# Kernel tuning notes

Hardware: AMD Instinct MI355X
Metric: run time of the kernel (lower is better)

The kernel has to match this reference:

```python
import jax, jax.numpy as jnp
import numpy as np

HEAD = 64

PARAM_NAMES = ['x_r','x_w','x_k','x_v','x_a','x_g','w0','w1','w2','a0','a1','a2',
               'v0','v1','v2','g1','g2','k_k','k_a','r_k','W_r','W_k','W_v','W_o',
               'ln_x_w','ln_x_b','ln1_w','ln1_b','ln2_w','ln2_b','c_x_k','W_ck','W_cv']


def token_shift(x):
    # previous token, zero-padded at t=0 (stateless shift state)
    return jnp.pad(x, ((0, 0), (1, 0), (0, 0)))[:, :-1]


def layer_norm(x, w, b, eps=1e-5):
    m = jnp.mean(x, -1, keepdims=True)
    v = jnp.mean(jnp.square(x - m), -1, keepdims=True)
    return (x - m) * jax.lax.rsqrt(v + eps) * w + b


def group_norm_heads(x, w, b, H, eps=64e-5):
    # GroupNorm(H, C) as used by RWKV7 ln_x (eps = head_size * 1e-5)
    B, T, C = x.shape
    xh = x.reshape(B, T, H, C // H)
    m = jnp.mean(xh, -1, keepdims=True)
    v = jnp.mean(jnp.square(xh - m), -1, keepdims=True)
    xh = (xh - m) * jax.lax.rsqrt(v + eps)
    return xh.reshape(B, T, C) * w + b


def wkv7(r, w, k, v, a, b):
    # r,w,k,v,a,b: [B,T,H,N]; w is per-channel decay in (0,1)
    # S_t = S_{t-1} * diag(w_t) + (S_{t-1} @ a_t) b_t^T + v_t k_t^T ; y_t = S_t @ r_t
    B, T, H, N = r.shape
    def step(S, inp):
        r_t, w_t, k_t, v_t, a_t, b_t = inp
        sa = jnp.einsum('bhij,bhj->bhi', S, a_t)
        S = S * w_t[:, :, None, :] + sa[..., None] * b_t[:, :, None, :] + v_t[..., None] * k_t[:, :, None, :]
        y = jnp.einsum('bhij,bhj->bhi', S, r_t)
        return S, y
    xs = tuple(jnp.moveaxis(t, 1, 0) for t in (r, w, k, v, a, b))
    S0 = jnp.zeros((B, H, N, N), r.dtype)
    _, ys = jax.lax.scan(step, S0, xs)
    return jnp.moveaxis(ys, 0, 1)


def time_mix(x, v_first, p, is_first_layer):
    B, T, C = x.shape
    H, N = C // HEAD, HEAD
    xx = token_shift(x) - x
    xr = x + xx * p['x_r']; xw = x + xx * p['x_w']; xk = x + xx * p['x_k']
    xv = x + xx * p['x_v']; xa = x + xx * p['x_a']; xg = x + xx * p['x_g']
    r = xr @ p['W_r']
    w = -jax.nn.softplus(-(p['w0'] + jnp.tanh(xw @ p['w1']) @ p['w2'])) - 0.5
    k = xk @ p['W_k']
    v = xv @ p['W_v']
    if is_first_layer:
        v_first = v
    else:
        v = v + (v_first - v) * jax.nn.sigmoid(p['v0'] + (xv @ p['v1']) @ p['v2'])
    a = jax.nn.sigmoid(p['a0'] + (xa @ p['a1']) @ p['a2'])  # in-context learning rate
    g = jax.nn.sigmoid(xg @ p['g1']) @ p['g2']
    kk = (k * p['k_k']).reshape(B, T, H, N)
    kk = kk / jnp.maximum(jnp.linalg.norm(kk, axis=-1, keepdims=True), 1e-12)
    k = k * (1.0 + (a - 1.0) * p['k_a'])
    decay = jnp.exp(-jnp.exp(w)).reshape(B, T, H, N)
    rh = r.reshape(B, T, H, N)
    kh = k.reshape(B, T, H, N)
    vh = v.reshape(B, T, H, N)
    ah = a.reshape(B, T, H, N)
    y = wkv7(rh, decay, kh, vh, -kk, kk * ah).reshape(B, T, C)
    y = group_norm_heads(y, p['ln_x_w'], p['ln_x_b'], H)
    bonus = jnp.sum(rh * kh * p['r_k'], -1, keepdims=True) * vh
    y = y + bonus.reshape(B, T, C)
    return (y * g) @ p['W_o'], v_first


def channel_mix(x, p):
    xx = token_shift(x) - x
    k = x + xx * p['c_x_k']
    k = jnp.square(jax.nn.relu(k @ p['W_ck']))
    return k @ p['W_cv']


def encoder_forward(x, params):
    L = params['W_r'].shape[0]
    v_first = None
    for i in range(L):
        p = {n: params[n][i] for n in PARAM_NAMES}
        att, v_first = time_mix(layer_norm(x, p['ln1_w'], p['ln1_b']), v_first, p, i == 0)
        x = x + att
        x = x + channel_mix(layer_norm(x, p['ln2_w'], p['ln2_b']), p)
    return x


def setup_inputs() -> dict:
    key = jax.random.key(0)
    L, B, T, C = 6, 2, 512, 768
    H, N = C // HEAD, HEAD
    Dw, Da, Dv, Dg, F = 64, 64, 32, 128, 4 * C
    keys = iter(jax.random.split(key, 48))
    def rn(shape, s):
        return jax.random.normal(next(keys), shape, jnp.float32) * s
    def ru(shape):
        return jax.random.uniform(next(keys), shape, jnp.float32)
    inp = {
        'x': rn((B, T, C), 1.0),
        'x_r': ru((L, C)), 'x_w': ru((L, C)), 'x_k': ru((L, C)),
        'x_v': ru((L, C)), 'x_a': ru((L, C)), 'x_g': ru((L, C)),
        'w0': rn((L, C), 0.3), 'w1': rn((L, C, Dw), 0.02), 'w2': rn((L, Dw, C), 0.02),
        'a0': rn((L, C), 0.1), 'a1': rn((L, C, Da), 0.02), 'a2': rn((L, Da, C), 0.02),
        'v0': rn((L, C), 0.1), 'v1': rn((L, C, Dv), 0.02), 'v2': rn((L, Dv, C), 0.02),
        'g1': rn((L, C, Dg), 0.02), 'g2': rn((L, Dg, C), 0.02),
        'k_k': 0.85 + rn((L, C), 0.05), 'k_a': 1.0 + rn((L, C), 0.05),
        'r_k': rn((L, H, N), 0.1),
        'W_r': rn((L, C, C), 0.02), 'W_k': rn((L, C, C), 0.02),
        'W_v': rn((L, C, C), 0.02), 'W_o': rn((L, C, C), 0.02),
        'ln_x_w': 1.0 + rn((L, C), 0.05), 'ln_x_b': rn((L, C), 0.05),
        'ln1_w': 1.0 + rn((L, C), 0.05), 'ln1_b': rn((L, C), 0.05),
        'ln2_w': 1.0 + rn((L, C), 0.05), 'ln2_b': rn((L, C), 0.05),
        'c_x_k': ru((L, C)),
        'W_ck': rn((L, C, F), 0.02), 'W_cv': rn((L, F, C), 0.02),
    }
    return inp


def reference(x, x_r, x_w, x_k, x_v, x_a, x_g, w0, w1, w2, a0, a1, a2, v0, v1, v2,
              g1, g2, k_k, k_a, r_k, W_r, W_k, W_v, W_o, ln_x_w, ln_x_b,
              ln1_w, ln1_b, ln2_w, ln2_b, c_x_k, W_ck, W_cv):
    params = dict(zip(PARAM_NAMES, (x_r, x_w, x_k, x_v, x_a, x_g, w0, w1, w2, a0, a1, a2,
                                    v0, v1, v2, g1, g2, k_k, k_a, r_k, W_r, W_k, W_v, W_o,
                                    ln_x_w, ln_x_b, ln1_w, ln1_b, ln2_w, ln2_b, c_x_k, W_ck, W_cv)))
    return encoder_forward(x, params)
```

## Files before the change

### kernel.cpp

```cpp
#include <hip/hip_runtime.h>
#include <hip/hip_bf16.h>
#include <math.h>

#define LAYERS 6
#define BBATCH 2
#define TT 512
#define CC 768
#define HH 12
#define MT (BBATCH*TT)
#define FF (4*CC)
#define LCH 32
#define NC (TT/LCH)
#define BH (BBATCH*HH)
#define SPAD 65

typedef __hip_bfloat16 bf16;
typedef __bf16 bf16x8 __attribute__((ext_vector_type(8)));
typedef float f32x4 __attribute__((ext_vector_type(4)));

__device__ inline bf16 f2b(float f) { return __float2bfloat16(f); }


__global__ __launch_bounds__(256) void copy_f(float* __restrict__ dst, const float* __restrict__ src) {
    size_t i = (size_t)blockIdx.x * 256 + threadIdx.x;
    dst[i] = src[i];
}


__global__ __launch_bounds__(256) void ln_shift_kernel(const float* __restrict__ x,
                                                       const float* __restrict__ w,
                                                       const float* __restrict__ b,
                                                       bf16* __restrict__ out) {
    int row = blockIdx.x;
    int t = row % TT;
    const float* xr = x + (size_t)row * CC;
    const float* xp = xr - CC;
    int tid = threadIdx.x;
    float c0 = xr[tid], c1 = xr[tid + 256], c2 = xr[tid + 512];
    float p0 = 0.f, p1 = 0.f, p2 = 0.f;
    if (t > 0) { p0 = xp[tid]; p1 = xp[tid + 256]; p2 = xp[tid + 512]; }
    float s  = c0 + c1 + c2, q  = c0 * c0 + c1 * c1 + c2 * c2;
    float sp = p0 + p1 + p2, qp = p0 * p0 + p1 * p1 + p2 * p2;
    for (int m = 1; m < 64; m <<= 1) {
        s += __shfl_xor(s, m); q += __shfl_xor(q, m);
        sp += __shfl_xor(sp, m); qp += __shfl_xor(qp, m);
    }
    __shared__ float rs[4], rq[4], rsp[4], rqp[4];
    int wid = tid >> 6;
    if ((tid & 63) == 0) { rs[wid] = s; rq[wid] = q; rsp[wid] = sp; rqp[wid] = qp; }
    __syncthreads();
    s  = rs[0] + rs[1] + rs[2] + rs[3];   q  = rq[0] + rq[1] + rq[2] + rq[3];
    sp = rsp[0] + rsp[1] + rsp[2] + rsp[3]; qp = rqp[0] + rqp[1] + rqp[2] + rqp[3];
    float meanC = s * (1.f / CC);
    float invC  = rsqrtf(q * (1.f / CC) - meanC * meanC + 1e-5f);
    float meanP = sp * (1.f / CC);
    float invP  = rsqrtf(qp * (1.f / CC) - meanP * meanP + 1e-5f);
    bf16* orow = out + (size_t)row * 1536;
    float cv[3] = {c0, c1, c2};
    float pv[3] = {p0, p1, p2};
#pragma unroll
    for (int j = 0; j < 3; ++j) {
        int cc = tid + j * 256;
        float lnc = (cv[j] - meanC) * invC * w[cc] + b[cc];
        float lnp = (t > 0) ? (pv[j] - meanP) * invP * w[cc] + b[cc] : 0.f;
        orow[cc] = f2b(lnc);
        orow[768 + cc] = f2b(lnp - lnc);
    }
}


struct CEntry { const float* W; const float* mix; bf16* dst; int Ksrc, Nsrc, Npad, Kdst, bstart; };
struct CArgs { CEntry e[14]; };

__global__ __launch_bounds__(256) void convert_weights(CArgs ca) {
    int bid = blockIdx.x;
    int idx = 0;
#pragma unroll
    for (int i = 1; i < 14; ++i) if (bid >= ca.e[i].bstart) idx = i;
    CEntry E = ca.e[idx];
    int t = bid - E.bstart;
    int ntN = E.Npad >> 5;
    int tn = (t % ntN) * 32, tk = (t / ntN) * 32;
    __shared__ float tile[32][33];
    int c = threadIdx.x & 31, r0 = threadIdx.x >> 5;
    int ks = tk;
    const float* mixp = nullptr;
    if (tk >= E.Ksrc) { ks = tk - E.Ksrc; mixp = E.mix; }
#pragma unroll
    for (int i = 0; i < 4; ++i) {
        int r = r0 + i * 8;
        float v = (tn + c < E.Nsrc) ? E.W[(size_t)(ks + r) * E.Nsrc + tn + c] : 0.f;
        if (mixp) v *= mixp[ks + r];
        tile[r][c] = v;
    }
    __syncthreads();
#pragma unroll
    for (int i = 0; i < 4; ++i) {
        int r = r0 + i * 8;
        E.dst[(size_t)(tn + r) * E.Kdst + tk + c] = f2b(tile[c][r]);
    }
}


struct EpiG {
    float* outF; bf16* outH;
    const float* p1; const float* p2;
    int epi, ld, ntrue;
};
struct EpiArgs { EpiG g[7]; int nb[8]; };

__device__ inline void epi_store(const EpiG& E, size_t idx, int lc, float v) {
    switch (E.epi) {
        case 0: E.outF[idx] = v; break;
        case 1: E.outH[idx] = f2b(v); break;
        case 2: E.outH[idx] = f2b(tanhf(v)); break;
        case 3: E.outH[idx] = f2b(1.f / (1.f + expf(-v))); break;
        case 4: { float t = fmaxf(v, 0.f); E.outH[idx] = f2b(t * t); } break;
        case 5: E.outF[idx] += v; break;
        case 6: { float z = E.p1[lc] + v; float nz = -z;
                  float sp = (nz > 20.f) ? nz : log1pf(expf(nz));
                  E.outF[idx] = expf(-expf(-sp - 0.5f)); } break;
        case 7: E.outF[idx] = 1.f / (1.f + expf(-(E.p1[lc] + v))); break;
        case 8: { float vv = E.outF[idx];
                  float s = 1.f / (1.f + expf(-(E.p1[lc] + v)));
                  E.outF[idx] = vv + (E.p2[idx] - vv) * s; } break;
    }
}


template<int BM, int BN>
__global__ __launch_bounds__(256) void gemm_multi(const __bf16* __restrict__ A,
                                                  const __bf16* __restrict__ Bt,
                                                  int K, EpiArgs ea) {
    constexpr int FM = BM / 32, FN = BN / 32;
    constexpr int ABYTES = BM * 64;
    constexpr int TOT = (BM + BN) * 64;
    constexpr int NCHUNK = TOT / 4096;
    __shared__ __align__(16) char smem[2][TOT];
    int tid = threadIdx.x;
    int lane = tid & 63, wid = tid >> 6;
    int bm = blockIdx.y * BM, bn = blockIdx.x * BN;
    int wm = (wid >> 1) * (BM / 2), wn = (wid & 1) * (BN / 2);
    f32x4 acc[FM][FN];
#pragma unroll
    for (int i = 0; i < FM; ++i)
#pragma unroll
        for (int j = 0; j < FN; ++j) acc[i][j] = (f32x4){0.f, 0.f, 0.f, 0.f};

    int nk = K >> 5;
    auto stage = [&](int buf, int k0) {
        char* sb = &smem[buf][0];
#pragma unroll
        for (int c = 0; c < NCHUNK; ++c) {
            int d = c * 4096 + tid * 16;
            int isB = d >= ABYTES;
            int dd = isB ? d - ABYTES : d;
            int row = dd >> 6;
            int u = (dd >> 4) & 3;
            int su = u ^ (row & 3);
            const __bf16* src = isB ? (Bt + (size_t)(bn + row) * K + k0 + su * 8)
                                    : (A  + (size_t)(bm + row) * K + k0 + su * 8);
            char* ldst = sb + c * 4096 + (tid & 192) * 16;
            __builtin_amdgcn_global_load_lds(
                (const __attribute__((address_space(1))) unsigned int*)src,
                (__attribute__((address_space(3))) unsigned int*)ldst, 16, 0, 0);
        }
    };

    stage(0, 0);
    __syncthreads();
    for (int t = 0; t < nk; ++t) {
        if (t + 1 < nk) stage((t + 1) & 1, (t + 1) * 32);
        const char* sA = &smem[t & 1][0];
        const char* sB = &smem[t & 1][ABYTES];
        int u = lane >> 4, r0 = lane & 15;
        bf16x8 af[FM], bfr[FN];
#pragma unroll
        for (int i = 0; i < FM; ++i) {
            int row = wm + i * 16 + r0;
            int su = u ^ (row & 3);
            af[i] = *(const bf16x8*)(sA + row * 64 + su * 16);
        }
#pragma unroll
        for (int j = 0; j < FN; ++j) {
            int row = wn + j * 16 + r0;
            int su = u ^ (row & 3);
            bfr[j] = *(const bf16x8*)(sB + row * 64 + su * 16);
        }
#pragma unroll
        for (int i = 0; i < FM; ++i)
#pragma unroll
            for (int j = 0; j < FN; ++j)
                acc[i][j] = __builtin_amdgcn_mfma_f32_16x16x32_bf16(af[i], bfr[j], acc[i][j], 0, 0, 0);
        __syncthreads();
    }

    int gid = 0;
#pragma unroll 1
    while (bn >= ea.nb[gid + 1]) ++gid;
    EpiG E = ea.g[gid];
    int colBase = ea.nb[gid];
#pragma unroll
    for (int i = 0; i < FM; ++i) {
#pragma unroll
        for (int j = 0; j < FN; ++j) {
#pragma unroll
            for (int q = 0; q < 4; ++q) {
                int gm = bm + wm + i * 16 + (lane >> 4) * 4 + q;
                int lc = bn + wn + j * 16 + (lane & 15) - colBase;
                if (lc < E.ntrue)
                    epi_store(E, (size_t)gm * E.ld + lc, lc, acc[i][j][q]);
            }
        }
    }
}


struct G2G { const __bf16* A; const __bf16* Bt; float* outF; const float* p1; const float* p2; int K; int epi; };
struct G2Args { G2G g[4]; };

template<int BM, int BN>
__global__ __launch_bounds__(256) void gemm_g2(G2Args ga) {
    G2G G = ga.g[blockIdx.z];
    const __bf16* A = G.A;
    const __bf16* Bt = G.Bt;
    int K = G.K;
    constexpr int FM = BM / 32, FN = BN / 32;
    constexpr int ABYTES = BM * 64;
    constexpr int TOT = (BM + BN) * 64;
    constexpr int NCHUNK = TOT / 4096;
    __shared__ __align__(16) char smem[2][TOT];
    int tid = threadIdx.x;
    int lane = tid & 63, wid = tid >> 6;
    int bm = blockIdx.y * BM, bn = blockIdx.x * BN;
    int wm = (wid >> 1) * (BM / 2), wn = (wid & 1) * (BN / 2);
    f32x4 acc[FM][FN];
#pragma unroll
    for (int i = 0; i < FM; ++i)
#pragma unroll
        for (int j = 0; j < FN; ++j) acc[i][j] = (f32x4){0.f, 0.f, 0.f, 0.f};

    int nk = K >> 5;
    auto stage = [&](int buf, int k0) {
        char* sb = &smem[buf][0];
#pragma unroll
        for (int c = 0; c < NCHUNK; ++c) {
            int d = c * 4096 + tid * 16;
            int isB = d >= ABYTES;
            int dd = isB ? d - ABYTES : d;
            int row = dd >> 6;
            int u = (dd >> 4) & 3;
            int su = u ^ (row & 3);
            const __bf16* src = isB ? (Bt + (size_t)(bn + row) * K + k0 + su * 8)
                                    : (A  + (size_t)(bm + row) * K + k0 + su * 8);
            char* ldst = sb + c * 4096 + (tid & 192) * 16;
            __builtin_amdgcn_global_load_lds(
                (const __attribute__((address_space(1))) unsigned int*)src,
                (__attribute__((address_space(3))) unsigned int*)ldst, 16, 0, 0);
        }
    };

    stage(0, 0);
    __syncthreads();
    for (int t = 0; t < nk; ++t) {
        if (t + 1 < nk) stage((t + 1) & 1, (t + 1) * 32);
        const char* sA = &smem[t & 1][0];
        const char* sB = &smem[t & 1][ABYTES];
        int u = lane >> 4, r0 = lane & 15;
        bf16x8 af[FM], bfr[FN];
#pragma unroll
        for (int i = 0; i < FM; ++i) {
            int row = wm + i * 16 + r0;
            int su = u ^ (row & 3);
            af[i] = *(const bf16x8*)(sA + row * 64 + su * 16);
        }
#pragma unroll
        for (int j = 0; j < FN; ++j) {
            int row = wn + j * 16 + r0;
            int su = u ^ (row & 3);
            bfr[j] = *(const bf16x8*)(sB + row * 64 + su * 16);
        }
#pragma unroll
        for (int i = 0; i < FM; ++i)
#pragma unroll
            for (int j = 0; j < FN; ++j)
                acc[i][j] = __builtin_amdgcn_mfma_f32_16x16x32_bf16(af[i], bfr[j], acc[i][j], 0, 0, 0);
        __syncthreads();
    }

    EpiG E;
    E.outF = G.outF; E.outH = nullptr; E.p1 = G.p1; E.p2 = G.p2;
    E.epi = G.epi; E.ld = 768; E.ntrue = 768;
#pragma unroll
    for (int i = 0; i < FM; ++i) {
#pragma unroll
        for (int j = 0; j < FN; ++j) {
#pragma unroll
            for (int q = 0; q < 4; ++q) {
                int gm = bm + wm + i * 16 + (lane >> 4) * 4 + q;
                int lc = bn + wn + j * 16 + (lane & 15);
                epi_store(E, (size_t)gm * 768 + lc, lc, acc[i][j][q]);
            }
        }
    }
}


__global__ __launch_bounds__(256) void chunkA_kernel(
    const float* __restrict__ r, const float* __restrict__ wd,
    const float* __restrict__ kraw, const float* __restrict__ av_,
    const float* __restrict__ v,
    const float* __restrict__ kkw, const float* __restrict__ kaw,
    float* __restrict__ kupd,
    float* __restrict__ yintra, float* __restrict__ zrO,
    float* __restrict__ mmO, float* __restrict__ zcO) {
    int c = blockIdx.x, bh = blockIdx.y;
    int b = bh / HH, h = bh % HH;
    __shared__ float Di[LCH][SPAD];
    __shared__ float Ah[LCH][SPAD];
    __shared__ float Bh[LCH][SPAD];
    __shared__ float Kh[LCH][SPAD];
    __shared__ float Rh[LCH][SPAD];
    __shared__ float Vt[LCH][SPAD];
    __shared__ float Qm[LCH][SPAD];
    __shared__ float Gba[LCH][LCH], Gka[LCH][LCH], Grb[LCH][LCH], Grk[LCH][LCH];
    int tid = threadIdx.x;
    int n = tid & 63, tq = tid >> 6;
    size_t base = ((size_t)(b * TT + c * LCH)) * CC + h * 64 + n;
    int cvec = h * 64 + n;
    float kkwv = kkw[cvec], kawv = kaw[cvec];
#pragma unroll
    for (int e = 0; e < 8; ++e) {
        int t = tq * 8 + e;
        size_t off = base + (size_t)t * CC;
        float kr = kraw[off];
        float aval = av_[off];
        float kk0 = kr * kkwv;
        float ss = kk0 * kk0;
        for (int m = 1; m < 64; m <<= 1) ss += __shfl_xor(ss, m);
        float rinv = 1.f / fmaxf(sqrtf(ss), 1e-12f);
        float kkv = kk0 * rinv;
        float ku = kr * (1.f + (aval - 1.f) * kawv);
        kupd[off] = ku;
        Di[t][n] = wd[off];
        Ah[t][n] = -kkv;
        Bh[t][n] = kkv * aval;
        Kh[t][n] = ku;
        Rh[t][n] = r[off];
        Vt[t][n] = v[off];
    }
    __syncthreads();
    if (tid < 64) {
        float d = 1.f;
        for (int t = 0; t < LCH; ++t) { d *= Di[t][tid]; Di[t][tid] = d; }
    }
    __syncthreads();
#pragma unroll
    for (int e = 0; e < 8; ++e) {
        int t = tq * 8 + e;
        float di = Di[t][n];
        float dp = (t == 0) ? 1.f : Di[t - 1][n];
        float inv = 1.f / di;
        Ah[t][n] *= dp;
        Bh[t][n] *= inv;
        Kh[t][n] *= inv;
        Rh[t][n] *= di;
    }
    __syncthreads();
    {
        int tp = tid >> 4, sp = tid & 15;
        int t0 = 2 * tp, s0 = 2 * sp;
        float gba00 = 0.f, gba01 = 0.f, gba10 = 0.f, gba11 = 0.f;
        float gka00 = 0.f, gka01 = 0.f, gka10 = 0.f, gka11 = 0.f;
        float grb00 = 0.f, grb01 = 0.f, grb10 = 0.f, grb11 = 0.f;
        float grk00 = 0.f, grk01 = 0.f, grk10 = 0.f, grk11 = 0.f;
#pragma unroll 4
        for (int j = 0; j < 64; ++j) {
            float a0 = Ah[t0][j], a1 = Ah[t0 + 1][j];
            float r0 = Rh[t0][j], r1 = Rh[t0 + 1][j];
            float b0 = Bh[s0][j], b1 = Bh[s0 + 1][j];
            float k0 = Kh[s0][j], k1 = Kh[s0 + 1][j];
            gba00 = fmaf(a0, b0, gba00); gba01 = fmaf(a0, b1, gba01);
            gba10 = fmaf(a1, b0, gba10); gba11 = fmaf(a1, b1, gba11);
            gka00 = fmaf(a0, k0, gka00); gka01 = fmaf(a0, k1, gka01);
            gka10 = fmaf(a1, k0, gka10); gka11 = fmaf(a1, k1, gka11);
            grb00 = fmaf(r0, b0, grb00); grb01 = fmaf(r0, b1, grb01);
            grb10 = fmaf(r1, b0, grb10); grb11 = fmaf(r1, b1, grb11);
            grk00 = fmaf(r0, k0, grk00); grk01 = fmaf(r0, k1, grk01);
            grk10 = fmaf(r1, k0, grk10); grk11 = fmaf(r1, k1, grk11);
        }
#pragma unroll
        for (int dt = 0; dt < 2; ++dt) {
            int t = t0 + dt;
#pragma unroll
            for (int ds = 0; ds < 2; ++ds) {
                int s = s0 + ds;
                float vba = dt ? (ds ? gba11 : gba10) : (ds ? gba01 : gba00);
                float vka = dt ? (ds ? gka11 : gka10) : (ds ? gka01 : gka00);
                float vrb = dt ? (ds ? grb11 : grb10) : (ds ? grb01 : grb00);
                float vrk = dt ? (ds ? grk11 : grk10) : (ds ? grk01 : grk00);
                Gba[t][s] = (s < t)  ? vba : 0.f;
                Gka[t][s] = (s < t)  ? vka : 0.f;
                Grb[t][s] = (s <= t) ? vrb : 0.f;
                Grk[t][s] = (s <= t) ? vrk : 0.f;
            }
        }
    }
    __syncthreads();
    {
        float acc[8];
#pragma unroll
        for (int e = 0; e < 8; ++e) acc[e] = 0.f;
        for (int s = 0; s < LCH; ++s) {
            float vs = Vt[s][n];
#pragma unroll
            for (int e = 0; e < 8; ++e)
                acc[e] = fmaf(Gka[tq * 8 + e][s], vs, acc[e]);
        }
#pragma unroll
        for (int e = 0; e < 8; ++e) Qm[tq * 8 + e][n] = acc[e];
    }
    __syncthreads();
    if (tq == 0) {
        for (int t = 1; t < LCH; ++t) {
            float acc = Ah[t][n];
            for (int s = 0; s < t; ++s) acc = fmaf(Gba[t][s], Ah[s][n], acc);
            Ah[t][n] = acc;
        }
    } else if (tq == 1) {
        for (int t = 1; t < LCH; ++t) {
            float acc = Qm[t][n];
            for (int s = 0; s < t; ++s) acc = fmaf(Gba[t][s], Qm[s][n], acc);
            Qm[t][n] = acc;
        }
    }
    __syncthreads();
    float dL_n = Di[LCH - 1][n];
    size_t obase = ((size_t)(bh * NC + c)) * LCH * 64;
    {
        float accY[8], accZ[8];
#pragma unroll
        for (int e = 0; e < 8; ++e) { accY[e] = 0.f; accZ[e] = Rh[tq * 8 + e][n]; }
        for (int s = 0; s < LCH; ++s) {
            float vs = Vt[s][n], qs = Qm[s][n], us = Ah[s][n];
#pragma unroll
            for (int e = 0; e < 8; ++e) {
                int t = tq * 8 + e;
                float grk_ = Grk[t][s], grb_ = Grb[t][s];
                accY[e] = fmaf(grk_, vs, fmaf(grb_, qs, accY[e]));
                accZ[e] = fmaf(grb_, us, accZ[e]);
            }
        }
#pragma unroll
        for (int e = 0; e < 8; ++e) {
            int t = tq * 8 + e;
            yintra[obase + t * 64 + n] = accY[e];
            zrO[obase + t * 64 + n] = accZ[e];
        }
    }
    {
        int pi = tid >> 4, ni = tid & 15;
        float accM[4][4], accZc[4][4];
#pragma unroll
        for (int dp = 0; dp < 4; ++dp)
#pragma unroll
            for (int dn = 0; dn < 4; ++dn) { accM[dp][dn] = 0.f; accZc[dp][dn] = 0.f; }
        for (int s = 0; s < LCH; ++s) {
            float aa[4], vv[4], qq[4], bb[4], kk[4];
#pragma unroll
            for (int d = 0; d < 4; ++d) {
                aa[d] = Ah[s][4 * pi + d];
                vv[d] = Vt[s][4 * pi + d];
                qq[d] = Qm[s][4 * pi + d];
                bb[d] = Bh[s][4 * ni + d];
                kk[d] = Kh[s][4 * ni + d];
            }
#pragma unroll
            for (int dp = 0; dp < 4; ++dp)
#pragma unroll
                for (int dn = 0; dn < 4; ++dn) {
                    accM[dp][dn]  = fmaf(aa[dp], bb[dn], accM[dp][dn]);
                    accZc[dp][dn] = fmaf(vv[dp], kk[dn], fmaf(qq[dp], bb[dn], accZc[dp][dn]));
                }
        }
        size_t mbase = ((size_t)(bh * NC + c)) * 4096;
        float dl[4];
#pragma unroll
        for (int dn = 0; dn < 4; ++dn) dl[dn] = Di[LCH - 1][4 * ni + dn];
#pragma unroll
        for (int dp = 0; dp < 4; ++dp) {
            int p = 4 * pi + dp;
            f32x4 m4, z4;
#pragma unroll
            for (int dn = 0; dn < 4; ++dn) {
                int nn = 4 * ni + dn;
                float mm = accM[dp][dn] + ((p == nn) ? 1.f : 0.f);
                m4[dn] = dl[dn] * mm;
                z4[dn] = dl[dn] * accZc[dp][dn];
            }
            *(f32x4*)(mmO + mbase + p * 64 + 4 * ni) = m4;
            *(f32x4*)(zcO + mbase + p * 64 + 4 * ni) = z4;
        }
    }
}


__global__ __launch_bounds__(256) void chunkB1_kernel(const float* __restrict__ mm,
                                                      const float* __restrict__ zc,
                                                      float* __restrict__ schk) {
    int bh = blockIdx.x;
    int tid = threadIdx.x;
    int i4 = tid >> 4, j4 = tid & 15;
    __shared__ float S[64][SPAD];
    __shared__ __align__(16) float Mb[2][64][64];
#pragma unroll
    for (int e = 0; e < 16; ++e) {
        int idx = tid + e * 256;
        S[idx >> 6][idx & 63] = 0.f;
    }
    const float* mbase = mm + (size_t)bh * NC * 4096;
    const float* zbase = zc + (size_t)bh * NC * 4096;
    float* sbase = schk + (size_t)bh * NC * 4096;
#pragma unroll
    for (int s = 0; s < 4; ++s) {
        __builtin_amdgcn_global_load_lds(
            (const __attribute__((address_space(1))) unsigned int*)(mbase + s * 1024 + tid * 4),
            (__attribute__((address_space(3))) unsigned int*)((char*)&Mb[0][0][0] + s * 4096 + (tid & 192) * 16),
            16, 0, 0);
    }
    f32x4 zcur[4], znxt[4];
#pragma unroll
    for (int d = 0; d < 4; ++d)
        zcur[d] = *(const f32x4*)(zbase + (i4 * 4 + d) * 64 + j4 * 4);
    __syncthreads();
#pragma unroll 1
    for (int c = 0; c < NC - 1; ++c) {
        int cb = c & 1;
        if (c < NC - 2) {
#pragma unroll
            for (int s = 0; s < 4; ++s) {
                __builtin_amdgcn_global_load_lds(
                    (const __attribute__((address_space(1))) unsigned int*)(mbase + (size_t)(c + 1) * 4096 + s * 1024 + tid * 4),
                    (__attribute__((address_space(3))) unsigned int*)((char*)&Mb[cb ^ 1][0][0] + s * 4096 + (tid & 192) * 16),
                    16, 0, 0);
            }
#pragma unroll
            for (int d = 0; d < 4; ++d)
                znxt[d] = *(const f32x4*)(zbase + (size_t)(c + 1) * 4096 + (i4 * 4 + d) * 64 + j4 * 4);
        }
        f32x4 acc0 = zcur[0], acc1 = zcur[1], acc2 = zcur[2], acc3 = zcur[3];
        for (int p = 0; p < 64; ++p) {
            f32x4 mrow = *(const f32x4*)&Mb[cb][p][j4 * 4];
            float s0 = S[i4 * 4 + 0][p];
            float s1 = S[i4 * 4 + 1][p];
            float s2 = S[i4 * 4 + 2][p];
            float s3 = S[i4 * 4 + 3][p];
#pragma unroll
            for (int u = 0; u < 4; ++u) {
                acc0[u] = fmaf(s0, mrow[u], acc0[u]);
                acc1[u] = fmaf(s1, mrow[u], acc1[u]);
                acc2[u] = fmaf(s2, mrow[u], acc2[u]);
                acc3[u] = fmaf(s3, mrow[u], acc3[u]);
            }
        }
        __syncthreads();
        float* cp = sbase + (size_t)(c + 1) * 4096;
#pragma unroll
        for (int u = 0; u < 4; ++u) {
            S[i4 * 4 + 0][j4 * 4 + u] = acc0[u];
            S[i4 * 4 + 1][j4 * 4 + u] = acc1[u];
            S[i4 * 4 + 2][j4 * 4 + u] = acc2[u];
            S[i4 * 4 + 3][j4 * 4 + u] = acc3[u];
        }
        *(f32x4*)(cp + (i4 * 4 + 0) * 64 + j4 * 4) = acc0;
        *(f32x4*)(cp + (i4 * 4 + 1) * 64 + j4 * 4) = acc1;
        *(f32x4*)(cp + (i4 * 4 + 2) * 64 + j4 * 4) = acc2;
        *(f32x4*)(cp + (i4 * 4 + 3) * 64 + j4 * 4) = acc3;
#pragma unroll
        for (int d = 0; d < 4; ++d) zcur[d] = znxt[d];
        __syncthreads();
    }
}


__global__ __launch_bounds__(256) void chunkY_kernel(
    const float* __restrict__ yintra, const float* __restrict__ zrI,
    const float* __restrict__ schk,
    const float* __restrict__ r, const float* __restrict__ kupd,
    const float* __restrict__ v, const float* __restrict__ g,
    const float* __restrict__ rk, const float* __restrict__ lw,
    const float* __restrict__ lb, bf16* __restrict__ out) {
    int c = blockIdx.x, bh = blockIdx.y;
    int b = bh / HH, h = bh % HH;
    __shared__ float Y[LCH][SPAD];
    __shared__ float Zr[LCH][SPAD];
    __shared__ float Sh[64][SPAD];
    int tid = threadIdx.x;
    int n = tid & 63, tq = tid >> 6;
    size_t obase = ((size_t)(bh * NC + c)) * LCH * 64;
#pragma unroll
    for (int e = 0; e < 8; ++e) {
        int idx = tid + e * 256;
        int row = idx >> 6, col = idx & 63;
        Y[row][col] = yintra[obase + idx];
        Zr[row][col] = zrI[obase + idx];
    }
    if (c > 0) {
        size_t sbase = ((size_t)(bh * NC + c)) * 4096;
#pragma unroll
        for (int e = 0; e < 16; ++e) {
            int idx = tid + e * 256;
            Sh[idx >> 6][idx & 63] = schk[sbase + idx];
        }
    }
    __syncthreads();
    if (c > 0) {
        float acc[8];
#pragma unroll
        for (int e = 0; e < 8; ++e) acc[e] = 0.f;
        for (int p = 0; p < 64; ++p) {
            float sv = Sh[n][p];
#pragma unroll
            for (int e = 0; e < 8; ++e)
                acc[e] = fmaf(Zr[tq * 8 + e][p], sv, acc[e]);
        }
#pragma unroll
        for (int e = 0; e < 8; ++e) Y[tq * 8 + e][n] += acc[e];
    }
    size_t rowbase = ((size_t)(b * TT + c * LCH)) * CC + h * 64 + n;
    float rkv = rk[h * 64 + n];
    float lwv = lw[h * 64 + n], lbv = lb[h * 64 + n];
#pragma unroll
    for (int e = 0; e < 8; ++e) {
        int t = tq * 8 + e;
        size_t off = rowbase + (size_t)t * CC;
        float yv = Y[t][n];
        float rv = r[off], kv = kupd[off], vv = v[off];
        float s1 = yv, s2 = yv * yv, s3 = rv * kv * rkv;
        for (int m = 1; m < 64; m <<= 1) {
            s1 += __shfl_xor(s1, m);
            s2 += __shfl_xor(s2, m);
            s3 += __shfl_xor(s3, m);
        }
        float mean = s1 * (1.f / 64.f);
        float var  = s2 * (1.f / 64.f) - mean * mean;
        float inv  = rsqrtf(var + 64e-5f);
        float val  = (yv - mean) * inv * lwv + lbv + s3 * vv;
        out[off] = f2b(val * g[off]);
    }
}


extern "C" void kernel_launch(void* const* d_in, const int* in_sizes, int n_in,
                              void* d_out, int out_size, void* d_ws, size_t ws_size,
                              hipStream_t stream) {
    (void)in_sizes; (void)n_in; (void)out_size;
    const float* x    = (const float*)d_in[0];
    const float* x_r  = (const float*)d_in[1];
    const float* x_w  = (const float*)d_in[2];
    const float* x_k  = (const float*)d_in[3];
    const float* x_v  = (const float*)d_in[4];
    const float* x_a  = (const float*)d_in[5];
    const float* x_g  = (const float*)d_in[6];
    const float* w0   = (const float*)d_in[7];
    const float* w1   = (const float*)d_in[8];
    const float* w2   = (const float*)d_in[9];
    const float* a0   = (const float*)d_in[10];
    const float* a1   = (const float*)d_in[11];
    const float* a2   = (const float*)d_in[12];
    const float* v0   = (const float*)d_in[13];
    const float* v1   = (const float*)d_in[14];
    const float* v2   = (const float*)d_in[15];
    const float* g1   = (const float*)d_in[16];
    const float* g2   = (const float*)d_in[17];
    const float* k_k  = (const float*)d_in[18];
    const float* k_a  = (const float*)d_in[19];
    const float* r_k  = (const float*)d_in[20];
    const float* W_r  = (const float*)d_in[21];
    const float* W_k  = (const float*)d_in[22];
    const float* W_v  = (const float*)d_in[23];
    const float* W_o  = (const float*)d_in[24];
    const float* ln_x_w = (const float*)d_in[25];
    const float* ln_x_b = (const float*)d_in[26];
    const float* ln1_w  = (const float*)d_in[27];
    const float* ln1_b  = (const float*)d_in[28];
    const float* ln2_w  = (const float*)d_in[29];
    const float* ln2_b  = (const float*)d_in[30];
    const float* c_x_k  = (const float*)d_in[31];
    const float* W_ck   = (const float*)d_in[32];
    const float* W_cv   = (const float*)d_in[33];

    const size_t MC = (size_t)MT * CC;
    char* wsb = (char*)d_ws;
    size_t woff = 0;
    auto alloc = [&](size_t bytes) -> void* {
        void* p = wsb + woff;
        woff += (bytes + 255) & ~(size_t)255;
        return p;
    };
    bf16* Bcat  = (bf16*)alloc((size_t)2624 * 1536 * 2);
    bf16* Bck   = (bf16*)alloc((size_t)3072 * 1536 * 2);
    bf16* w2t   = (bf16*)alloc((size_t)768 * 64 * 2);
    bf16* a2t   = (bf16*)alloc((size_t)768 * 64 * 2);
    bf16* v2t   = (bf16*)alloc((size_t)768 * 32 * 2);
    bf16* g2t   = (bf16*)alloc((size_t)768 * 128 * 2);
    bf16* Wo_t  = (bf16*)alloc((size_t)768 * 768 * 2);
    bf16* Wcv_t = (bf16*)alloc((size_t)768 * 3072 * 2);
    bf16* A1    = (bf16*)alloc((size_t)MT * 1536 * 2);
    float* rbuf  = (float*)alloc(MC * 4);
    float* kraw  = (float*)alloc(MC * 4);
    float* kupd  = (float*)alloc(MC * 4);
    float* vbuf  = (float*)alloc(MC * 4);
    float* vfirst= (float*)alloc(MC * 4);
    float* abuf  = (float*)alloc(MC * 4);
    float* dbuf  = (float*)alloc(MC * 4);
    float* gbuf  = (float*)alloc(MC * 4);
    bf16* w1o   = (bf16*)alloc((size_t)MT * 64 * 2);
    bf16* a1o   = (bf16*)alloc((size_t)MT * 64 * 2);
    bf16* v1o   = (bf16*)alloc((size_t)MT * 32 * 2);
    bf16* g1o   = (bf16*)alloc((size_t)MT * 128 * 2);
    bf16* hbuf  = (bf16*)alloc((size_t)MT * FF * 2);
    bf16* ghout = (bf16*)alloc(MC * 2);
    float* yintraW = (float*)alloc((size_t)BH * NC * LCH * 64 * 4);
    float* zrW     = (float*)alloc((size_t)BH * NC * LCH * 64 * 4);
    float* mmW     = (float*)alloc((size_t)BH * NC * 4096 * 4);
    float* zcW     = (float*)alloc((size_t)BH * NC * 4096 * 4);
    float* schkW   = (float*)alloc((size_t)BH * NC * 4096 * 4);
    if (woff > ws_size) return;

    float* xcur = (float*)d_out;
    copy_f<<<MC / 256, 256, 0, stream>>>(xcur, x);

    for (int l = 0; l < LAYERS; ++l) {
        size_t oC = (size_t)l * CC;
        float* vptr = (l == 0) ? vfirst : vbuf;

        CArgs ca;
        ca.e[0]  = {W_r  + (size_t)l * 589824, x_r + oC, Bcat,               768, 768, 768, 1536, 0};
        ca.e[1]  = {W_k  + (size_t)l * 589824, x_k + oC, Bcat + (size_t)768  * 1536, 768, 768, 768, 1536, 0};
        ca.e[2]  = {W_v  + (size_t)l * 589824, x_v + oC, Bcat + (size_t)1536 * 1536, 768, 768, 768, 1536, 0};
        ca.e[3]  = {w1   + (size_t)l * 49152,  x_w + oC, Bcat + (size_t)2304 * 1536, 768, 64, 64, 1536, 0};
        ca.e[4]  = {a1   + (size_t)l * 49152,  x_a + oC, Bcat + (size_t)2368 * 1536, 768, 64, 64, 1536, 0};
        ca.e[5]  = {g1   + (size_t)l * 98304,  x_g + oC, Bcat + (size_t)2432 * 1536, 768, 128, 128, 1536, 0};
        ca.e[6]  = {v1   + (size_t)l * 24576,  x_v + oC, Bcat + (size_t)2560 * 1536, 768, 32, 64, 1536, 0};
        ca.e[7]  = {W_ck + (size_t)l * 2359296, c_x_k + oC, Bck, 768, 3072, 3072, 1536, 0};
        ca.e[8]  = {w2   + (size_t)l * 49152,  nullptr, w2t,   64, 768, 768, 64, 0};
        ca.e[9]  = {a2   + (size_t)l * 49152,  nullptr, a2t,   64, 768, 768, 64, 0};
        ca.e[10] = {v2   + (size_t)l * 24576,  nullptr, v2t,   32, 768, 768, 32, 0};
        ca.e[11] = {g2   + (size_t)l * 98304,  nullptr, g2t,  128, 768, 768, 128, 0};
        ca.e[12] = {W_o  + (size_t)l * 589824, nullptr, Wo_t, 768, 768, 768, 768, 0};
        ca.e[13] = {W_cv + (size_t)l * 2359296, nullptr, Wcv_t, 3072, 768, 768, 3072, 0};
        int btot = 0;
        for (int i = 0; i < 14; ++i) {
            ca.e[i].bstart = btot;
            btot += (ca.e[i].Npad >> 5) * (ca.e[i].Kdst >> 5);
        }
        convert_weights<<<btot, 256, 0, stream>>>(ca);

        ln_shift_kernel<<<MT, 256, 0, stream>>>(xcur, ln1_w + oC, ln1_b + oC, A1);

        EpiArgs e1;
        e1.g[0] = {rbuf,  nullptr, nullptr, nullptr, 0, 768, 768};
        e1.g[1] = {kraw,  nullptr, nullptr, nullptr, 0, 768, 768};
        e1.g[2] = {vptr,  nullptr, nullptr, nullptr, 0, 768, 768};
        e1.g[3] = {nullptr, w1o, nullptr, nullptr, 2, 64, 64};
        e1.g[4] = {nullptr, a1o, nullptr, nullptr, 1, 64, 64};
        e1.g[5] = {nullptr, g1o, nullptr, nullptr, 3, 128, 128};
        e1.g[6] = {nullptr, v1o, nullptr, nullptr, 1, 32, 32};
        int nb1[8] = {0, 768, 1536, 2304, 2368, 2432, 2560, 2624};
        for (int i = 0; i < 8; ++i) e1.nb[i] = nb1[i];
        gemm_multi<128, 64><<<dim3(41, 8), 256, 0, stream>>>((const __bf16*)A1, (const __bf16*)Bcat, 1536, e1);

        G2Args g2a;
        g2a.g[0] = {(const __bf16*)w1o, (const __bf16*)w2t, dbuf, w0 + oC, nullptr, 64, 6};
        g2a.g[1] = {(const __bf16*)a1o, (const __bf16*)a2t, abuf, a0 + oC, nullptr, 64, 7};
        g2a.g[2] = {(const __bf16*)g1o, (const __bf16*)g2t, gbuf, nullptr, nullptr, 128, 0};
        g2a.g[3] = {(const __bf16*)v1o, (const __bf16*)v2t, vbuf, v0 + oC, vfirst, 32, 8};
        gemm_g2<128, 64><<<dim3(12, 8, (l == 0) ? 3 : 4), 256, 0, stream>>>(g2a);

        chunkA_kernel<<<dim3(NC, BH), 256, 0, stream>>>(rbuf, dbuf, kraw, abuf, vptr,
                                                        k_k + oC, k_a + oC, kupd,
                                                        yintraW, zrW, mmW, zcW);
        chunkB1_kernel<<<BH, 256, 0, stream>>>(mmW, zcW, schkW);
        chunkY_kernel<<<dim3(NC, BH), 256, 0, stream>>>(yintraW, zrW, schkW,
                                                        rbuf, kupd, vptr, gbuf,
                                                        r_k + (size_t)l * 768,
                                                        ln_x_w + oC, ln_x_b + oC, ghout);

        EpiArgs eo;
        eo.g[0] = {xcur, nullptr, nullptr, nullptr, 5, 768, 768};
        eo.nb[0] = 0; for (int i = 1; i < 8; ++i) eo.nb[i] = 1 << 30;
        eo.nb[1] = 768;
        gemm_multi<64, 64><<<dim3(12, 16), 256, 0, stream>>>((const __bf16*)ghout, (const __bf16*)Wo_t, 768, eo);

        ln_shift_kernel<<<MT, 256, 0, stream>>>(xcur, ln2_w + oC, ln2_b + oC, A1);

        EpiArgs ec;
        ec.g[0] = {nullptr, hbuf, nullptr, nullptr, 4, 3072, 3072};
        ec.nb[0] = 0; for (int i = 1; i < 8; ++i) ec.nb[i] = 1 << 30;
        ec.nb[1] = 3072;
        gemm_multi<128, 64><<<dim3(48, 8), 256, 0, stream>>>((const __bf16*)A1, (const __bf16*)Bck, 1536, ec);

        EpiArgs ev;
        ev.g[0] = {xcur, nullptr, nullptr, nullptr, 5, 768, 768};
        ev.nb[0] = 0; for (int i = 1; i < 8; ++i) ev.nb[i] = 1 << 30;
        ev.nb[1] = 768;
        gemm_multi<64, 64><<<dim3(12, 16), 256, 0, stream>>>((const __bf16*)hbuf, (const __bf16*)Wcv_t, 3072, ev);
    }
}
```

Measured before the change: 1.546 ms.

## Run inter-chunk state recurrence on MFMA with split-bf16 precision

The serial chunk-state scan in chunkB1 now uses bf16 MFMA instructions instead of scalar FP32 FMAs. It keeps near-fp32 accuracy by splitting both operands into high and low bf16 parts and summing three products. chunkA now writes the transition matrix transposed as hi/lo bf16 pairs, and chunkB1 prefetches it into registers instead of staging it through LDS. This shortens the latency-bound sequential loop, which runs on only 24 blocks, but trades some precision and register pressure for it.

```diff
diff --git a/kernel.cpp b/kernel.cpp
--- a/kernel.cpp
+++ b/kernel.cpp
@@ -16,9 +16,17 @@
 
 typedef __hip_bfloat16 bf16;
 typedef __bf16 bf16x8 __attribute__((ext_vector_type(8)));
+typedef __bf16 bf16x4 __attribute__((ext_vector_type(4)));
 typedef float f32x4 __attribute__((ext_vector_type(4)));
 
 __device__ inline bf16 f2b(float f) { return __float2bfloat16(f); }
+__device__ inline __bf16 f2bb(float f) {
+    __hip_bfloat16 h = __float2bfloat16(f);
+    return __builtin_bit_cast(__bf16, h);
+}
+__device__ inline float bb2f(__bf16 h) {
+    return __bfloat162float(__builtin_bit_cast(__hip_bfloat16, h));
+}
 
 
 __global__ __launch_bounds__(256) void copy_f(float* __restrict__ dst, const float* __restrict__ src) {
@@ -313,7 +321,8 @@
     const float* __restrict__ kkw, const float* __restrict__ kaw,
     float* __restrict__ kupd,
     float* __restrict__ yintra, float* __restrict__ zrO,
-    float* __restrict__ mmO, float* __restrict__ zcO) {
+    __bf16* __restrict__ mtHi, __bf16* __restrict__ mtLo,
+    float* __restrict__ zcO) {
     int c = blockIdx.x, bh = blockIdx.y;
     int b = bh / HH, h = bh % HH;
     __shared__ float Di[LCH][SPAD];
@@ -435,7 +444,6 @@
         }
     }
     __syncthreads();
-    float dL_n = Di[LCH - 1][n];
     size_t obase = ((size_t)(bh * NC + c)) * LCH * 64;
     {
         float accY[8], accZ[8];
@@ -490,94 +498,121 @@
 #pragma unroll
         for (int dp = 0; dp < 4; ++dp) {
             int p = 4 * pi + dp;
-            f32x4 m4, z4;
-#pragma unroll
-            for (int dn = 0; dn < 4; ++dn) {
-                int nn = 4 * ni + dn;
-                float mm = accM[dp][dn] + ((p == nn) ? 1.f : 0.f);
-                m4[dn] = dl[dn] * mm;
-                z4[dn] = dl[dn] * accZc[dp][dn];
-            }
-            *(f32x4*)(mmO + mbase + p * 64 + 4 * ni) = m4;
+            f32x4 z4;
+#pragma unroll
+            for (int dn = 0; dn < 4; ++dn) z4[dn] = dl[dn] * accZc[dp][dn];
             *(f32x4*)(zcO + mbase + p * 64 + 4 * ni) = z4;
         }
-    }
-}
-
-
-__global__ __launch_bounds__(256) void chunkB1_kernel(const float* __restrict__ mm,
-                                                      const float* __restrict__ zc,
-                                                      float* __restrict__ schk) {
+#pragma unroll
+        for (int dn = 0; dn < 4; ++dn) {
+            int nn = 4 * ni + dn;
+            float dlv = dl[dn];
+            bf16x4 h4, l4;
+#pragma unroll
+            for (int dp = 0; dp < 4; ++dp) {
+                int p = 4 * pi + dp;
+                float mm = (accM[dp][dn] + ((p == nn) ? 1.f : 0.f)) * dlv;
+                __bf16 hb = f2bb(mm);
+                h4[dp] = hb;
+                l4[dp] = f2bb(mm - bb2f(hb));
+            }
+            *(bf16x4*)(mtHi + mbase + (size_t)nn * 64 + 4 * pi) = h4;
+            *(bf16x4*)(mtLo + mbase + (size_t)nn * 64 + 4 * pi) = l4;
+        }
+    }
+}
+
+
+__global__ __launch_bounds__(256) void chunkB1_kernel(
+    const float* __restrict__ zc,
+    const __bf16* __restrict__ mtHi,
+    const __bf16* __restrict__ mtLo,
+    float* __restrict__ schk) {
     int bh = blockIdx.x;
     int tid = threadIdx.x;
-    int i4 = tid >> 4, j4 = tid & 15;
-    __shared__ float S[64][SPAD];
-    __shared__ __align__(16) float Mb[2][64][64];
-#pragma unroll
-    for (int e = 0; e < 16; ++e) {
-        int idx = tid + e * 256;
-        S[idx >> 6][idx & 63] = 0.f;
-    }
-    const float* mbase = mm + (size_t)bh * NC * 4096;
+    int lane = tid & 63, w = tid >> 6;
+    int r0 = lane & 15, u = lane >> 4;
+    __shared__ __align__(16) float S[64][68];
+    for (int i = tid; i < 64 * 68; i += 256) (&S[0][0])[i] = 0.f;
     const float* zbase = zc + (size_t)bh * NC * 4096;
+    const __bf16* hbase = mtHi + (size_t)bh * NC * 4096;
+    const __bf16* lbase = mtLo + (size_t)bh * NC * 4096;
     float* sbase = schk + (size_t)bh * NC * 4096;
-#pragma unroll
-    for (int s = 0; s < 4; ++s) {
-        __builtin_amdgcn_global_load_lds(
-            (const __attribute__((address_space(1))) unsigned int*)(mbase + s * 1024 + tid * 4),
-            (__attribute__((address_space(3))) unsigned int*)((char*)&Mb[0][0][0] + s * 4096 + (tid & 192) * 16),
-            16, 0, 0);
-    }
-    f32x4 zcur[4], znxt[4];
-#pragma unroll
-    for (int d = 0; d < 4; ++d)
-        zcur[d] = *(const f32x4*)(zbase + (i4 * 4 + d) * 64 + j4 * 4);
+    int arow = w * 16 + r0;
+
+    bf16x8 mh[2][4][2], ml[2][4][2];
+    f32x4 zf[2][4];
+#pragma unroll
+    for (int ct = 0; ct < 4; ++ct) {
+#pragma unroll
+        for (int ks = 0; ks < 2; ++ks) {
+            size_t mo = (size_t)(ct * 16 + r0) * 64 + ks * 32 + u * 8;
+            mh[0][ct][ks] = *(const bf16x8*)(hbase + mo);
+            ml[0][ct][ks] = *(const bf16x8*)(lbase + mo);
+        }
+#pragma unroll
+        for (int q = 0; q < 4; ++q)
+            zf[0][ct][q] = zbase[(size_t)(w * 16 + u * 4 + q) * 64 + ct * 16 + r0];
+    }
     __syncthreads();
 #pragma unroll 1
     for (int c = 0; c < NC - 1; ++c) {
         int cb = c & 1;
-        if (c < NC - 2) {
-#pragma unroll
-            for (int s = 0; s < 4; ++s) {
-                __builtin_amdgcn_global_load_lds(
-                    (const __attribute__((address_space(1))) unsigned int*)(mbase + (size_t)(c + 1) * 4096 + s * 1024 + tid * 4),
-                    (__attribute__((address_space(3))) unsigned int*)((char*)&Mb[cb ^ 1][0][0] + s * 4096 + (tid & 192) * 16),
-                    16, 0, 0);
-            }
-#pragma unroll
-            for (int d = 0; d < 4; ++d)
-                znxt[d] = *(const f32x4*)(zbase + (size_t)(c + 1) * 4096 + (i4 * 4 + d) * 64 + j4 * 4);
-        }
-        f32x4 acc0 = zcur[0], acc1 = zcur[1], acc2 = zcur[2], acc3 = zcur[3];
-        for (int p = 0; p < 64; ++p) {
-            f32x4 mrow = *(const f32x4*)&Mb[cb][p][j4 * 4];
-            float s0 = S[i4 * 4 + 0][p];
-            float s1 = S[i4 * 4 + 1][p];
-            float s2 = S[i4 * 4 + 2][p];
-            float s3 = S[i4 * 4 + 3][p];
-#pragma unroll
-            for (int u = 0; u < 4; ++u) {
-                acc0[u] = fmaf(s0, mrow[u], acc0[u]);
-                acc1[u] = fmaf(s1, mrow[u], acc1[u]);
-                acc2[u] = fmaf(s2, mrow[u], acc2[u]);
-                acc3[u] = fmaf(s3, mrow[u], acc3[u]);
+        if (c + 1 < NC - 1) {
+            const __bf16* hn = hbase + (size_t)(c + 1) * 4096;
+            const __bf16* ln = lbase + (size_t)(c + 1) * 4096;
+            const float* zn = zbase + (size_t)(c + 1) * 4096;
+#pragma unroll
+            for (int ct = 0; ct < 4; ++ct) {
+#pragma unroll
+                for (int ks = 0; ks < 2; ++ks) {
+                    size_t mo = (size_t)(ct * 16 + r0) * 64 + ks * 32 + u * 8;
+                    mh[cb ^ 1][ct][ks] = *(const bf16x8*)(hn + mo);
+                    ml[cb ^ 1][ct][ks] = *(const bf16x8*)(ln + mo);
+                }
+#pragma unroll
+                for (int q = 0; q < 4; ++q)
+                    zf[cb ^ 1][ct][q] = zn[(size_t)(w * 16 + u * 4 + q) * 64 + ct * 16 + r0];
+            }
+        }
+        bf16x8 ah[2], al[2];
+#pragma unroll
+        for (int ks = 0; ks < 2; ++ks) {
+            f32x4 s0 = *(const f32x4*)&S[arow][ks * 32 + u * 8];
+            f32x4 s1 = *(const f32x4*)&S[arow][ks * 32 + u * 8 + 4];
+#pragma unroll
+            for (int e = 0; e < 4; ++e) {
+                __bf16 h0 = f2bb(s0[e]);
+                ah[ks][e] = h0;
+                al[ks][e] = f2bb(s0[e] - bb2f(h0));
+                __bf16 h1 = f2bb(s1[e]);
+                ah[ks][4 + e] = h1;
+                al[ks][4 + e] = f2bb(s1[e] - bb2f(h1));
+            }
+        }
+        f32x4 acc[4];
+#pragma unroll
+        for (int ct = 0; ct < 4; ++ct) {
+            acc[ct] = zf[cb][ct];
+#pragma unroll
+            for (int ks = 0; ks < 2; ++ks) {
+                acc[ct] = __builtin_amdgcn_mfma_f32_16x16x32_bf16(ah[ks], mh[cb][ct][ks], acc[ct], 0, 0, 0);
+                acc[ct] = __builtin_amdgcn_mfma_f32_16x16x32_bf16(ah[ks], ml[cb][ct][ks], acc[ct], 0, 0, 0);
+                acc[ct] = __builtin_amdgcn_mfma_f32_16x16x32_bf16(al[ks], mh[cb][ct][ks], acc[ct], 0, 0, 0);
             }
         }
         __syncthreads();
         float* cp = sbase + (size_t)(c + 1) * 4096;
 #pragma unroll
-        for (int u = 0; u < 4; ++u) {
-            S[i4 * 4 + 0][j4 * 4 + u] = acc0[u];
-            S[i4 * 4 + 1][j4 * 4 + u] = acc1[u];
-            S[i4 * 4 + 2][j4 * 4 + u] = acc2[u];
-            S[i4 * 4 + 3][j4 * 4 + u] = acc3[u];
-        }
-        *(f32x4*)(cp + (i4 * 4 + 0) * 64 + j4 * 4) = acc0;
-        *(f32x4*)(cp + (i4 * 4 + 1) * 64 + j4 * 4) = acc1;
-        *(f32x4*)(cp + (i4 * 4 + 2) * 64 + j4 * 4) = acc2;
-        *(f32x4*)(cp + (i4 * 4 + 3) * 64 + j4 * 4) = acc3;
-#pragma unroll
-        for (int d = 0; d < 4; ++d) zcur[d] = znxt[d];
+        for (int ct = 0; ct < 4; ++ct) {
+#pragma unroll
+            for (int q = 0; q < 4; ++q) {
+                int row = w * 16 + u * 4 + q;
+                int col = ct * 16 + r0;
+                S[row][col] = acc[ct][q];
+                cp[(size_t)row * 64 + col] = acc[ct][q];
+            }
+        }
         __syncthreads();
     }
 }
@@ -723,7 +758,8 @@
     bf16* ghout = (bf16*)alloc(MC * 2);
     float* yintraW = (float*)alloc((size_t)BH * NC * LCH * 64 * 4);
     float* zrW     = (float*)alloc((size_t)BH * NC * LCH * 64 * 4);
-    float* mmW     = (float*)alloc((size_t)BH * NC * 4096 * 4);
+    __bf16* mtHiW  = (__bf16*)alloc((size_t)BH * NC * 4096 * 2);
+    __bf16* mtLoW  = (__bf16*)alloc((size_t)BH * NC * 4096 * 2);
     float* zcW     = (float*)alloc((size_t)BH * NC * 4096 * 4);
     float* schkW   = (float*)alloc((size_t)BH * NC * 4096 * 4);
     if (woff > ws_size) return;
@@ -780,8 +816,8 @@
 
         chunkA_kernel<<<dim3(NC, BH), 256, 0, stream>>>(rbuf, dbuf, kraw, abuf, vptr,
                                                         k_k + oC, k_a + oC, kupd,
-                                                        yintraW, zrW, mmW, zcW);
-        chunkB1_kernel<<<BH, 256, 0, stream>>>(mmW, zcW, schkW);
+                                                        yintraW, zrW, mtHiW, mtLoW, zcW);
+        chunkB1_kernel<<<BH, 256, 0, stream>>>(zcW, mtHiW, mtLoW, schkW);
         chunkY_kernel<<<dim3(NC, BH), 256, 0, stream>>>(yintraW, zrW, schkW,
                                                         rbuf, kupd, vptr, gbuf,
                                                         r_k + (size_t)l * 768,
```

Measured after the change: 1.744 ms. +12.8%, slower.
